# Kernel optimization log

Hardware: AMD Instinct MI355X
Metric: run time of the kernel (lower is better)

The kernel has to match this reference:

```python
import jax, jax.numpy as jnp
import numpy as np
import math

EMBED_DIM = 1024
NUM_HEADS = 16
HEAD_DIM = EMBED_DIM // NUM_HEADS
SCALE = 1.0 / math.sqrt(HEAD_DIM)


def setup_inputs() -> dict:
    key = jax.random.key(0)
    ks = jax.random.split(key, 11)
    B, S, E = 4, 2048, EMBED_DIM
    lim = 1.0 / math.sqrt(E)
    def lin(k):
        kw, kb = jax.random.split(k)
        W = jax.random.uniform(kw, (E, E), jnp.float32, -lim, lim)
        b = jax.random.uniform(kb, (E,), jnp.float32, -lim, lim)
        return W, b
    Wq, bq = lin(ks[0])
    Wk, bk = lin(ks[1])
    Wv, bv = lin(ks[2])
    Wo, bo = lin(ks[3])
    query = jax.random.normal(ks[4], (B, S, E), jnp.float32)
    key_t = jax.random.normal(ks[5], (B, S, E), jnp.float32)
    value = jax.random.normal(ks[6], (B, S, E), jnp.float32)
    return {"query": query, "key": key_t, "value": value,
            "Wq": Wq, "bq": bq, "Wk": Wk, "bk": bk,
            "Wv": Wv, "bv": bv, "Wo": Wo, "bo": bo}


def reference(query, key, value, Wq, bq, Wk, bk, Wv, bv, Wo, bo):
    B, S, E = query.shape
    H, D = NUM_HEADS, HEAD_DIM
    # nn.Linear: x @ W^T + b; reshape to (B, H, S, D)
    def proj(x, W, b):
        return (x @ W.T + b).reshape(B, S, H, D).transpose(0, 2, 1, 3)
    q = proj(query, Wq, bq)
    k = proj(key, Wk, bk)
    v = proj(value, Wv, bv)
    scores = jnp.einsum('bhsd,bhtd->bhst', q, k) * SCALE  # [B,H,S,S]
    attn = jax.nn.softmax(scores, axis=-1)
    # dropout is identity in eval/reference mode
    attended = jnp.einsum('bhst,bhtd->bhsd', attn, v)
    attended = attended.transpose(0, 2, 1, 3).reshape(B, S, E)
    out = attended @ Wo.T + bo
    return out, attn
```

## Files before the change

### kernel.cpp

```cpp
#include <hip/hip_runtime.h>
#include <hip/hip_bf16.h>

typedef __attribute__((ext_vector_type(8))) short short8;
typedef __attribute__((ext_vector_type(4))) float f32x4;
typedef unsigned short u16;
typedef unsigned int u32;

#define AS1 __attribute__((address_space(1)))
#define AS3 __attribute__((address_space(3)))

__device__ __forceinline__ void cp16(const void* g, void* l) {
  __builtin_amdgcn_global_load_lds((const AS1 u32*)g, (AS3 u32*)l, 16, 0, 0);
}

__device__ __forceinline__ u16 f2bf(float x) {
  union { float f; unsigned u; } c; c.f = x;
  unsigned u = c.u;
  unsigned r = (u + 0x7fffu + ((u >> 16) & 1u)) >> 16;
  return (u16)r;
}

__device__ __forceinline__ u32 pk2bf(float a, float b) {
  __hip_bfloat162 h = __float22bfloat162_rn(float2{a, b});
  union { __hip_bfloat162 h; u32 u; } c; c.h = h; return c.u;
}

__device__ __forceinline__ short8 cvt8(float4 x0, float4 x1) {
  short8 v;
  v[0]=(short)f2bf(x0.x); v[1]=(short)f2bf(x0.y); v[2]=(short)f2bf(x0.z); v[3]=(short)f2bf(x0.w);
  v[4]=(short)f2bf(x1.x); v[5]=(short)f2bf(x1.y); v[6]=(short)f2bf(x1.z); v[7]=(short)f2bf(x1.w);
  return v;
}

__global__ __launch_bounds__(256) void cvt_all(
    const float* __restrict__ q, const float* __restrict__ k, const float* __restrict__ v,
    const float* __restrict__ wq, const float* __restrict__ wk,
    const float* __restrict__ wv, const float* __restrict__ wo,
    u16* __restrict__ Xb, u16* __restrict__ Wb)
{
  const int TOT = 3670016;
  for (int c = blockIdx.x * 256 + threadIdx.x; c < TOT; c += gridDim.x * 256) {
    const float* s; u16* d;
    if (c < 3145728) {
      int z = c >> 20, off = c & 1048575;
      s = ((z == 0) ? q : (z == 1) ? k : v) + (size_t)off * 8;
      d = Xb + (size_t)c * 8;
    } else {
      int wc = c - 3145728;
      int z = wc >> 17, off = wc & 131071;
      s = ((z == 0) ? wq : (z == 1) ? wk : (z == 2) ? wv : wo) + (size_t)off * 8;
      d = Wb + (size_t)wc * 8;
    }
    float4 a = ((const float4*)s)[0], b = ((const float4*)s)[1];
    *(short8*)d = cvt8(a, b);
  }
}

template<int SWAP>
__device__ __forceinline__ void gemm_core_bf16(const u16* __restrict__ A,
                                               const u16* __restrict__ B,
                                               u16* As, u16* Bs,
                                               f32x4 acc[4][4])
{
  const int tid = threadIdx.x;
  const int lane = tid & 63, wid = tid >> 6;
  const int lo = lane & 15, hi = lane >> 4;
  const int wr0 = (wid >> 1) * 64, wc0 = (wid & 1) * 64;

  for (int k0 = 0; k0 < 1024; k0 += 64) {
    __syncthreads();
#pragma unroll
    for (int it = 0; it < 4; ++it) {
      int idx = it * 256 + tid;
      int row = idx >> 3, slot = idx & 7;
      cp16(A + (size_t)row * 1024 + k0 + slot * 8, As + (size_t)idx * 8);
      cp16(B + (size_t)row * 1024 + k0 + slot * 8, Bs + (size_t)idx * 8);
    }
    __syncthreads();
#pragma unroll
    for (int kk = 0; kk < 2; ++kk) {
      short8 af[4], bfr[4];
      int slot = kk * 4 + hi;
#pragma unroll
      for (int i = 0; i < 4; ++i)
        af[i] = *(const short8*)(&As[(wr0 + i * 16 + lo) * 64 + slot * 8]);
#pragma unroll
      for (int j = 0; j < 4; ++j)
        bfr[j] = *(const short8*)(&Bs[(wc0 + j * 16 + lo) * 64 + slot * 8]);
#pragma unroll
      for (int i = 0; i < 4; ++i)
#pragma unroll
        for (int j = 0; j < 4; ++j)
          acc[i][j] = SWAP
            ? __builtin_amdgcn_mfma_f32_16x16x32_bf16(bfr[j], af[i], acc[i][j], 0, 0, 0)
            : __builtin_amdgcn_mfma_f32_16x16x32_bf16(af[i], bfr[j], acc[i][j], 0, 0, 0);
    }
  }
}

__global__ __launch_bounds__(256) void gemm_qkv(
    const u16* __restrict__ Xb, const u16* __restrict__ Wb,
    const float* __restrict__ bq, const float* __restrict__ bk, const float* __restrict__ bv,
    u16* __restrict__ Qh, u16* __restrict__ Kh, u16* __restrict__ Vt)
{
  __shared__ __align__(16) u16 As[128 * 64];
  __shared__ __align__(16) u16 Bs[128 * 64];
  const int bid = blockIdx.x;
  const int w = (bid & 7) * 192 + (bid >> 3);
  const int z = w / 512, r = w % 512;
  const int bm0 = (r >> 3) * 128, bn0 = (r & 7) * 128;
  const u16* A = Xb + (size_t)z * 8388608 + (size_t)bm0 * 1024;
  const u16* W = Wb + (size_t)z * 1048576 + (size_t)bn0 * 1024;
  const float* bias = (z == 0) ? bq : (z == 1) ? bk : bv;

  f32x4 acc[4][4] = {};
  if (z < 2) gemm_core_bf16<0>(A, W, As, Bs, acc);
  else       gemm_core_bf16<1>(A, W, As, Bs, acc);

  const int lane = threadIdx.x & 63, wid = threadIdx.x >> 6;
  const int lo = lane & 15, hi = lane >> 4;
  const int wr0 = (wid >> 1) * 64, wc0 = (wid & 1) * 64;

  if (z < 2) {
    u16* out = (z == 0) ? Qh : Kh;
    const float sc = (z == 0) ? 0.125f * 1.44269504088896f : 1.0f;
#pragma unroll
    for (int j = 0; j < 4; ++j) {
      int n = bn0 + wc0 + j * 16 + lo;
      float bb = bias[n];
      int h = n >> 6, d = n & 63;
#pragma unroll
      for (int i = 0; i < 4; ++i)
#pragma unroll
        for (int r2 = 0; r2 < 4; ++r2) {
          int m = bm0 + wr0 + i * 16 + hi * 4 + r2;
          int b = m >> 11, s = m & 2047;
          float v = (acc[i][j][r2] + bb) * sc;
          out[(((size_t)(b * 16 + h)) * 2048 + s) * 64 + d] = f2bf(v);
        }
    }
  } else {
#pragma unroll
    for (int j = 0; j < 4; ++j) {
#pragma unroll
      for (int r2 = 0; r2 < 4; ++r2) {
        int n = bn0 + wc0 + j * 16 + hi * 4 + r2;
        float bb = bias[n];
        int h = n >> 6, d = n & 63;
#pragma unroll
        for (int i = 0; i < 4; ++i) {
          int m = bm0 + wr0 + i * 16 + lo;
          int b = m >> 11, s = m & 2047;
          Vt[(((size_t)(b * 16 + h)) * 64 + d) * 2048 + s] = f2bf(acc[i][j][r2] + bb);
        }
      }
    }
  }
}

__global__ __launch_bounds__(256) void gemm_out(
    const u16* __restrict__ ATT, const u16* __restrict__ Wo,
    const float* __restrict__ bo, float* __restrict__ out)
{
  __shared__ __align__(16) u16 As[128 * 64];
  __shared__ __align__(16) u16 Bs[128 * 64];
  const int bid = blockIdx.x;
  const int w = (bid & 7) * 64 + (bid >> 3);
  const int bm0 = (w >> 3) * 128, bn0 = (w & 7) * 128;
  f32x4 acc[4][4] = {};
  gemm_core_bf16<0>(ATT + (size_t)bm0 * 1024, Wo + (size_t)bn0 * 1024, As, Bs, acc);

  const int lane = threadIdx.x & 63, wid = threadIdx.x >> 6;
  const int lo = lane & 15, hi = lane >> 4;
  const int wr0 = (wid >> 1) * 64, wc0 = (wid & 1) * 64;
#pragma unroll
  for (int j = 0; j < 4; ++j) {
    int n = bn0 + wc0 + j * 16 + lo;
    float bb = bo[n];
#pragma unroll
    for (int i = 0; i < 4; ++i)
#pragma unroll
      for (int r = 0; r < 4; ++r) {
        int m = bm0 + wr0 + i * 16 + hi * 4 + r;
        out[(size_t)m * 1024 + n] = acc[i][j][r] + bb;
      }
  }
}

#define C2 11.5415603f
__global__ __launch_bounds__(256) void attn_fused(
    const u16* __restrict__ Qh, const u16* __restrict__ Kh,
    const u16* __restrict__ Vt, float* __restrict__ attnOut,
    u16* __restrict__ ATT)
{
  __shared__ __align__(16) u16 Ks[2][64 * 64];
  __shared__ __align__(16) u16 Vs[2][64 * 64];
  __shared__ __align__(16) u16 Ps[64 * 64];
  const int tid = threadIdx.x, lane = tid & 63, wid = tid >> 6;
  const int lo = lane & 15, hi = lane >> 4;
  const int bid = blockIdx.x;
  const int xcd = bid & 7, idx = bid >> 3;
  const int bh = xcd * 8 + (idx >> 5);
  const int q0 = (idx & 31) * 64;
  const int wq0 = wid * 16;
  const int qr = wq0 + lo;

  const u16* Qg  = Qh + ((size_t)bh * 2048 + q0) * 64;
  const u16* Kg0 = Kh + (size_t)bh * 2048 * 64;
  const u16* Vg0 = Vt + (size_t)bh * 64 * 2048;

  const int srow0 = tid >> 3,         sslot0 = tid & 7;
  const int srow1 = (256 + tid) >> 3, sslot1 = tid & 7;
  const int dst0 = srow0 * 64 + ((sslot0 ^ (srow0 & 7)) << 3);
  const int dst1 = srow1 * 64 + ((sslot1 ^ (srow1 & 7)) << 3);

  short8 qa[2];
#pragma unroll
  for (int kk = 0; kk < 2; ++kk)
    qa[kk] = *(const short8*)(Qg + qr * 64 + (kk * 4 + hi) * 8);

  {
    short8 k0 = *(const short8*)(Kg0 + (size_t)srow0 * 64 + sslot0 * 8);
    short8 k1 = *(const short8*)(Kg0 + (size_t)srow1 * 64 + sslot1 * 8);
    *(short8*)(&Ks[0][dst0]) = k0;
    *(short8*)(&Ks[0][dst1]) = k1;
  }
  __syncthreads();
  float lsum = 0.f;
  for (int kt = 0; kt < 32; ++kt) {
    const int cur = kt & 1;
    short8 kn0, kn1;
    if (kt < 31) {
      const u16* Kn = Kg0 + (size_t)(kt + 1) * 4096;
      kn0 = *(const short8*)(Kn + (size_t)srow0 * 64 + sslot0 * 8);
      kn1 = *(const short8*)(Kn + (size_t)srow1 * 64 + sslot1 * 8);
    }
    f32x4 sc[4] = {};
#pragma unroll
    for (int kk = 0; kk < 2; ++kk) {
      int slot = kk * 4 + hi;
#pragma unroll
      for (int j = 0; j < 4; ++j) {
        int row = j * 16 + lo;
        short8 kb = *(const short8*)(&Ks[cur][row * 64 + ((slot ^ (row & 7)) << 3)]);
        sc[j] = __builtin_amdgcn_mfma_f32_16x16x32_bf16(kb, qa[kk], sc[j], 0, 0, 0);
      }
    }
#pragma unroll
    for (int j = 0; j < 4; ++j)
#pragma unroll
      for (int r = 0; r < 4; ++r) lsum += __builtin_amdgcn_exp2f(sc[j][r] - C2);
    if (kt < 31) {
      *(short8*)(&Ks[cur ^ 1][dst0]) = kn0;
      *(short8*)(&Ks[cur ^ 1][dst1]) = kn1;
    }
    __syncthreads();
  }
  lsum += __shfl_xor(lsum, 16);
  lsum += __shfl_xor(lsum, 32);
  const float shift2 = C2 + __builtin_amdgcn_logf(lsum);

  {
    short8 k0 = *(const short8*)(Kg0 + (size_t)srow0 * 64 + sslot0 * 8);
    short8 k1 = *(const short8*)(Kg0 + (size_t)srow1 * 64 + sslot1 * 8);
    short8 v0 = *(const short8*)(Vg0 + (size_t)srow0 * 2048 + sslot0 * 8);
    short8 v1 = *(const short8*)(Vg0 + (size_t)srow1 * 2048 + sslot1 * 8);
    *(short8*)(&Ks[0][dst0]) = k0;  *(short8*)(&Ks[0][dst1]) = k1;
    *(short8*)(&Vs[0][dst0]) = v0;  *(short8*)(&Vs[0][dst1]) = v1;
  }
  __syncthreads();
  f32x4 oacc[4] = {};
  for (int kt = 0; kt < 32; ++kt) {
    const int cur = kt & 1;
    const int t0 = kt * 64;
    short8 kn0, kn1, vn0, vn1;
    if (kt < 31) {
      const u16* Kn = Kg0 + (size_t)(kt + 1) * 4096;
      kn0 = *(const short8*)(Kn + (size_t)srow0 * 64 + sslot0 * 8);
      kn1 = *(const short8*)(Kn + (size_t)srow1 * 64 + sslot1 * 8);
      vn0 = *(const short8*)(Vg0 + (size_t)srow0 * 2048 + (t0 + 64) + sslot0 * 8);
      vn1 = *(const short8*)(Vg0 + (size_t)srow1 * 2048 + (t0 + 64) + sslot1 * 8);
    }
    f32x4 sc[4] = {};
#pragma unroll
    for (int kk = 0; kk < 2; ++kk) {
      int slot = kk * 4 + hi;
#pragma unroll
      for (int j = 0; j < 4; ++j) {
        int row = j * 16 + lo;
        short8 kb = *(const short8*)(&Ks[cur][row * 64 + ((slot ^ (row & 7)) << 3)]);
        sc[j] = __builtin_amdgcn_mfma_f32_16x16x32_bf16(kb, qa[kk], sc[j], 0, 0, 0);
      }
    }
    float p[4][4];
#pragma unroll
    for (int j = 0; j < 4; ++j)
#pragma unroll
      for (int r = 0; r < 4; ++r) p[j][r] = __builtin_amdgcn_exp2f(sc[j][r] - shift2);

    float* aOut = attnOut + ((size_t)bh * 2048 + q0 + qr) * 2048 + t0 + hi * 4;
#pragma unroll
    for (int j = 0; j < 4; ++j) {
      f32x4 f4;
      f4[0] = p[j][0]; f4[1] = p[j][1]; f4[2] = p[j][2]; f4[3] = p[j][3];
      __builtin_nontemporal_store(f4, (f32x4*)(aOut + j * 16));
    }
#pragma unroll
    for (int j = 0; j < 4; ++j) {
      int byte = (qr * 128 + j * 32 + hi * 8) ^ ((qr & 7) << 4);
      uint2 uu; uu.x = pk2bf(p[j][0], p[j][1]); uu.y = pk2bf(p[j][2], p[j][3]);
      *(uint2*)((char*)Ps + byte) = uu;
    }
#pragma unroll
    for (int c = 0; c < 2; ++c) {
      int byte = (qr * 128 + c * 64 + hi * 16) ^ ((qr & 7) << 4);
      short8 pa = *(const short8*)((char*)Ps + byte);
      int slot = c * 4 + hi;
#pragma unroll
      for (int j = 0; j < 4; ++j) {
        int vrow = j * 16 + lo;
        short8 vb = *(const short8*)(&Vs[cur][vrow * 64 + ((slot ^ (vrow & 7)) << 3)]);
        oacc[j] = __builtin_amdgcn_mfma_f32_16x16x32_bf16(pa, vb, oacc[j], 0, 0, 0);
      }
    }
    if (kt < 31) {
      *(short8*)(&Ks[cur ^ 1][dst0]) = kn0;
      *(short8*)(&Ks[cur ^ 1][dst1]) = kn1;
      *(short8*)(&Vs[cur ^ 1][dst0]) = vn0;
      *(short8*)(&Vs[cur ^ 1][dst1]) = vn1;
    }
    __syncthreads();
  }
  const int b = bh >> 4, h = bh & 15;
#pragma unroll
  for (int j = 0; j < 4; ++j)
#pragma unroll
    for (int r = 0; r < 4; ++r) {
      int ql = wq0 + hi * 4 + r;
      int d = j * 16 + lo;
      size_t row = (size_t)b * 2048 + q0 + ql;
      ATT[row * 1024 + h * 64 + d] = f2bf(oacc[j][r]);
    }
}

extern "C" void kernel_launch(void* const* d_in, const int* in_sizes, int n_in,
                              void* d_out, int out_size, void* d_ws, size_t ws_size,
                              hipStream_t stream) {
  const float* query = (const float*)d_in[0];
  const float* key   = (const float*)d_in[1];
  const float* value = (const float*)d_in[2];
  const float* Wq = (const float*)d_in[3];
  const float* bq = (const float*)d_in[4];
  const float* Wk = (const float*)d_in[5];
  const float* bk = (const float*)d_in[6];
  const float* Wv = (const float*)d_in[7];
  const float* bv = (const float*)d_in[8];
  const float* Wo = (const float*)d_in[9];
  const float* bo = (const float*)d_in[10];

  u16* Xb  = (u16*)d_ws;
  u16* Wb  = Xb + 25165824;
  u16* Qh  = Wb + 4194304;
  u16* Kh  = Qh + 8388608;
  u16* Vt  = Kh + 8388608;
  u16* ATT = Xb;

  float* outO  = (float*)d_out;
  float* attnO = outO + (size_t)8388608;

  cvt_all<<<2048, 256, 0, stream>>>(query, key, value, Wq, Wk, Wv, Wo, Xb, Wb);
  gemm_qkv<<<1536, 256, 0, stream>>>(Xb, Wb, bq, bk, bv, Qh, Kh, Vt);
  attn_fused<<<2048, 256, 0, stream>>>(Qh, Kh, Vt, attnO, ATT);
  gemm_out<<<512, 256, 0, stream>>>(ATT, Wb + 3145728, bo, outO);
}
```

Measured before the change: 439.5 us.

## Replace LDS round-trip for P with permlane swaps; raise priority around MFMAs

Removes the shared-memory staging buffer for the bf16 probability tile and instead rearranges the packed P values across lanes in registers with v_permlane32/16_swap so they match the MFMA A-operand layout. This eliminates an LDS write and read per tile, plus the Ps allocation, which may raise occupancy. It also wraps the MFMA loops in s_setprio to favour matrix issue over other waves. Correctness depends on the permlane sequence exactly reproducing the previous transposed layout.

```diff
diff --git a/kernel.cpp b/kernel.cpp
--- a/kernel.cpp
+++ b/kernel.cpp
@@ -195,7 +195,6 @@
 {
   __shared__ __align__(16) u16 Ks[2][64 * 64];
   __shared__ __align__(16) u16 Vs[2][64 * 64];
-  __shared__ __align__(16) u16 Ps[64 * 64];
   const int tid = threadIdx.x, lane = tid & 63, wid = tid >> 6;
   const int lo = lane & 15, hi = lane >> 4;
   const int bid = blockIdx.x;
@@ -236,6 +235,7 @@
       kn1 = *(const short8*)(Kn + (size_t)srow1 * 64 + sslot1 * 8);
     }
     f32x4 sc[4] = {};
+    __builtin_amdgcn_s_setprio(1);
 #pragma unroll
     for (int kk = 0; kk < 2; ++kk) {
       int slot = kk * 4 + hi;
@@ -246,6 +246,7 @@
         sc[j] = __builtin_amdgcn_mfma_f32_16x16x32_bf16(kb, qa[kk], sc[j], 0, 0, 0);
       }
     }
+    __builtin_amdgcn_s_setprio(0);
 #pragma unroll
     for (int j = 0; j < 4; ++j)
 #pragma unroll
@@ -282,6 +283,7 @@
       vn1 = *(const short8*)(Vg0 + (size_t)srow1 * 2048 + (t0 + 64) + sslot1 * 8);
     }
     f32x4 sc[4] = {};
+    __builtin_amdgcn_s_setprio(1);
 #pragma unroll
     for (int kk = 0; kk < 2; ++kk) {
       int slot = kk * 4 + hi;
@@ -292,6 +294,7 @@
         sc[j] = __builtin_amdgcn_mfma_f32_16x16x32_bf16(kb, qa[kk], sc[j], 0, 0, 0);
       }
     }
+    __builtin_amdgcn_s_setprio(0);
     float p[4][4];
 #pragma unroll
     for (int j = 0; j < 4; ++j)
@@ -305,23 +308,32 @@
       f4[0] = p[j][0]; f4[1] = p[j][1]; f4[2] = p[j][2]; f4[3] = p[j][3];
       __builtin_nontemporal_store(f4, (f32x4*)(aOut + j * 16));
     }
+    u32 w01[4], w23[4];
 #pragma unroll
     for (int j = 0; j < 4; ++j) {
-      int byte = (qr * 128 + j * 32 + hi * 8) ^ ((qr & 7) << 4);
-      uint2 uu; uu.x = pk2bf(p[j][0], p[j][1]); uu.y = pk2bf(p[j][2], p[j][3]);
-      *(uint2*)((char*)Ps + byte) = uu;
+      w01[j] = pk2bf(p[j][0], p[j][1]);
+      w23[j] = pk2bf(p[j][2], p[j][3]);
     }
 #pragma unroll
     for (int c = 0; c < 2; ++c) {
-      int byte = (qr * 128 + c * 64 + hi * 16) ^ ((qr & 7) << 4);
-      short8 pa = *(const short8*)((char*)Ps + byte);
+      u32 U = w01[c * 2], V = w01[c * 2 + 1];
+      u32 S = w23[c * 2], T = w23[c * 2 + 1];
+      asm volatile("v_permlane32_swap_b32 %0, %1" : "+v"(U), "+v"(V));
+      asm volatile("v_permlane16_swap_b32 %0, %1" : "+v"(U), "+v"(V));
+      asm volatile("v_permlane32_swap_b32 %0, %1" : "+v"(S), "+v"(T));
+      asm volatile("v_permlane16_swap_b32 %0, %1" : "+v"(S), "+v"(T));
+      short8 pa;
+      ((u32*)&pa)[0] = U; ((u32*)&pa)[1] = S;
+      ((u32*)&pa)[2] = V; ((u32*)&pa)[3] = T;
       int slot = c * 4 + hi;
-#pragma unroll
-      for (int j = 0; j < 4; ++j) {
-        int vrow = j * 16 + lo;
+      __builtin_amdgcn_s_setprio(1);
+#pragma unroll
+      for (int j4 = 0; j4 < 4; ++j4) {
+        int vrow = j4 * 16 + lo;
         short8 vb = *(const short8*)(&Vs[cur][vrow * 64 + ((slot ^ (vrow & 7)) << 3)]);
-        oacc[j] = __builtin_amdgcn_mfma_f32_16x16x32_bf16(pa, vb, oacc[j], 0, 0, 0);
-      }
+        oacc[j4] = __builtin_amdgcn_mfma_f32_16x16x32_bf16(pa, vb, oacc[j4], 0, 0, 0);
+      }
+      __builtin_amdgcn_s_setprio(0);
     }
     if (kt < 31) {
       *(short8*)(&Ks[cur ^ 1][dst0]) = kn0;
```

Result: no change. 439.6 us (+0.0%).
